# Kernel optimization log

Hardware: AMD Instinct MI355X
Metric: run time of the kernel (lower is better)

Reference implementation:

```python
import jax, jax.numpy as jnp
import numpy as np
from jax import lax

N, H, W, C = 4, 256, 256, 128
COUT = 128
BS_IN, BS_OUT, BSTR = 18, 16, 16  # gather block, conv-out block, block stride
N_ACTIVE = 512


def setup_inputs() -> dict:
    key = jax.random.key(0)
    ks = jax.random.split(key, 8)
    x = jax.random.normal(ks[0], (N, H, W, C), dtype=jnp.float32)
    w = jax.random.normal(ks[1], (3, 3, C, COUT), dtype=jnp.float32) * 0.05  # HWIO
    b = jax.random.normal(ks[2], (COUT,), dtype=jnp.float32) * 0.05
    gamma = jax.random.uniform(ks[3], (COUT,), dtype=jnp.float32, minval=0.5, maxval=1.5)
    beta = jax.random.normal(ks[4], (COUT,), dtype=jnp.float32) * 0.1
    mean = jax.random.normal(ks[5], (COUT,), dtype=jnp.float32) * 0.1
    var = jax.random.uniform(ks[6], (COUT,), dtype=jnp.float32, minval=0.5, maxval=1.5)
    # unique active block ids over the N x (H/16) x (W/16) grid -> disjoint scatter targets
    n_blocks = N * (H // BSTR) * (W // BSTR)
    active = jax.random.permutation(ks[7], n_blocks)[:N_ACTIVE].astype(jnp.int32)
    return {"x": x, "w": w, "b": b, "gamma": gamma, "beta": beta,
            "mean": mean, "var": var, "active": active}


def reference(x, w, b, gamma, beta, mean, var, active):
    n_, h_, w_, c_ = x.shape
    nby, nbx = h_ // BSTR, w_ // BSTR
    bn = active // (nby * nbx)
    rem = active % (nby * nbx)
    by = rem // nbx
    bx = rem % nbx

    # --- sparse_gather: overlapping BS_IN x BS_IN input blocks (zero-pad edges) ---
    pad = BS_IN - BS_OUT
    xp = jnp.pad(x, ((0, 0), (0, pad), (0, pad), (0, 0)))
    Hp, Wp = h_ + pad, w_ + pad
    d_in = jnp.arange(BS_IN, dtype=jnp.int32)
    hs = by[:, None] * BSTR + d_in[None, :]            # [Nb, 18]
    ws = bx[:, None] * BSTR + d_in[None, :]            # [Nb, 18]
    gidx = bn[:, None, None] * (Hp * Wp) + hs[:, :, None] * Wp + ws[:, None, :]
    p = xp.reshape(-1, c_)[gidx]                       # [Nb, 18, 18, C]

    # --- dense conv + BN(eval, eps=1e-3) + ReLU on gathered blocks ---
    q = lax.conv_general_dilated(p, w, window_strides=(1, 1), padding='VALID',
                                 dimension_numbers=('NHWC', 'HWIO', 'NHWC'))
    q = q + b
    q = (q - mean) * (gamma * lax.rsqrt(var + 1e-3)) + beta
    q = jax.nn.relu(q)                                 # [Nb, 16, 16, COUT]

    # --- sparse_scatter: write disjoint BS_OUT blocks back into a copy of x ---
    d_out = jnp.arange(BS_OUT, dtype=jnp.int32)
    hso = by[:, None] * BSTR + d_out[None, :]
    wso = bx[:, None] * BSTR + d_out[None, :]
    sidx = bn[:, None, None] * (h_ * w_) + hso[:, :, None] * w_ + wso[:, None, :]
    y = x.reshape(-1, c_).at[sidx.reshape(-1)].set(q.reshape(-1, q.shape[-1]))
    return y.reshape(n_, h_, w_, c_)
```

## Files before the change

kernel.cpp:

```cpp
#include <hip/hip_runtime.h>
#include <hip/hip_bf16.h>

#define H_ 256
#define W_ 256
#define C_ 128
#define NBPOS 1024
#define NACT 512

typedef __bf16 bf16x8 __attribute__((ext_vector_type(8)));
typedef float f32x4 __attribute__((ext_vector_type(4)));

#define SCALE_OFF 294912
#define SHIFT_OFF 295424
#define INACT_OFF 295936

#define LGKM_BARRIER() do { \
  asm volatile("s_waitcnt lgkmcnt(0)" ::: "memory"); \
  __builtin_amdgcn_s_barrier(); \
  __builtin_amdgcn_sched_barrier(0); \
} while (0)

__global__ void prep_kernel(const float* __restrict__ w, const float* __restrict__ b,
                            const float* __restrict__ gamma, const float* __restrict__ beta,
                            const float* __restrict__ mean, const float* __restrict__ var,
                            const int* __restrict__ active,
                            __bf16* __restrict__ wprep, float* __restrict__ scale,
                            float* __restrict__ shift, int* __restrict__ inact) {
  int blk = blockIdx.x, tid = threadIdx.x;
  if (blk < 576) {
    int o = blk * 256 + tid;
    int j = o & 7, cout = (o >> 3) & 127, k8 = (o >> 10) & 15, tap = o >> 14;
    wprep[o] = (__bf16)w[((size_t)tap * 128 + k8 * 8 + j) * 128 + cout];
    return;
  }
  __shared__ unsigned mask[32];
  __shared__ int cnt;
  if (tid < 32) mask[tid] = 0u;
  if (tid == 0) cnt = 0;
  __syncthreads();
  for (int i = tid; i < NACT; i += 256) {
    int a = active[i];
    atomicOr(&mask[a >> 5], 1u << (a & 31));
  }
  if (tid < 128) {
    float s = gamma[tid] * rsqrtf(var[tid] + 1e-3f);
    scale[tid] = s;
    shift[tid] = (b[tid] - mean[tid]) * s + beta[tid];
  }
  __syncthreads();
  for (int p = tid; p < NBPOS; p += 256) {
    if (!((mask[p >> 5] >> (p & 31)) & 1u)) {
      int q = atomicAdd(&cnt, 1);
      inact[q] = p;
    }
  }
}

__global__ __launch_bounds__(256, 2) void main_kernel(
    const float* __restrict__ x, const __bf16* __restrict__ wprep,
    const float* __restrict__ scale, const float* __restrict__ shift,
    const int* __restrict__ active, const int* __restrict__ inact,
    float* __restrict__ y) {
  __shared__ unsigned char ldsA[324 * 128];
  __shared__ unsigned char ldsB[2][8192];

  const int tid = threadIdx.x;
  const int lane = tid & 63;
  const int wid = tid >> 6;

  const int aid = active[blockIdx.x];
  const int bn = aid >> 8, by = (aid >> 4) & 15, bx = aid & 15;
  const int h0 = by * 16, w0 = bx * 16;
  const float* xb = x + (size_t)bn * (H_ * W_ * C_);

  const int cid = inact[blockIdx.x];
  const size_t cbase4 =
      ((((size_t)(cid >> 8) * H_ + ((cid >> 4) & 15) * 16) * W_ + (cid & 15) * 16) * C_) >> 2;
  const f32x4* __restrict__ xs = (const f32x4*)x;
  f32x4* __restrict__ ys = (f32x4*)y;
  f32x4 cbuf[4];
  auto cidx = [&](int c) -> size_t {
    int lin = (c << 8) + tid;
    return cbase4 + (size_t)(lin >> 9) * (W_ * C_ / 4) + (lin & 511);
  };

  f32x4 acc[4][8];
  f32x4 zero = {0.f, 0.f, 0.f, 0.f};
#pragma unroll
  for (int i = 0; i < 4; ++i)
#pragma unroll
    for (int jj = 0; jj < 8; ++jj) acc[i][jj] = zero;

  const uint4* wp4 = (const uint4*)wprep;
  uint4 t0, t1;
  auto load_t = [&](int u) {
    int ks = u % 18, h = u / 18;
    int tile = ((ks >> 1) << 2) + (h << 1) + (ks & 1);
    t0 = wp4[tile * 512 + tid];
    t1 = wp4[tile * 512 + 256 + tid];
  };
  auto stage = [&](int half) {
    for (int u = tid; u < 324 * 8; u += 256) {
      int s = u >> 3, c8 = u & 7;
      int iy = s / 18, ix = s - iy * 18;
      int hs = h0 + iy, wsp = w0 + ix;
      float4 f0 = make_float4(0.f, 0.f, 0.f, 0.f), f1 = f0;
      if (hs < H_ && wsp < W_) {
        const float* p = xb + (size_t)(hs * W_ + wsp) * C_ + half * 64 + c8 * 8;
        f0 = *(const float4*)p;
        f1 = *(const float4*)(p + 4);
      }
      bf16x8 v;
      v[0] = (__bf16)f0.x; v[1] = (__bf16)f0.y; v[2] = (__bf16)f0.z; v[3] = (__bf16)f0.w;
      v[4] = (__bf16)f1.x; v[5] = (__bf16)f1.y; v[6] = (__bf16)f1.z; v[7] = (__bf16)f1.w;
      int lin = s * 128 + c8 * 16;
      *(bf16x8*)(&ldsA[lin ^ ((s & 7) << 4)]) = v;
    }
  };

  cbuf[0] = xs[cidx(0)];
  cbuf[1] = xs[cidx(1)];
  load_t(0);
  stage(0);
  ((uint4*)ldsB[0])[tid] = t0;
  ((uint4*)ldsB[0])[256 + tid] = t1;
  load_t(1);
  LGKM_BARRIER();

  const int koff = (lane >> 4) * 16;
  const int colb = (lane & 15) * 16;
  const int krow = (lane >> 4) * 2048;

#pragma unroll 4
  for (int u = 0; u < 36; ++u) {
    const int cur = u & 1;

    if (u < 32) __builtin_nontemporal_store(cbuf[u & 3], &ys[cidx(u)]);
    if (u < 30) cbuf[(u + 2) & 3] = xs[cidx(u + 2)];

    if (u < 35) {
      ((uint4*)ldsB[cur ^ 1])[tid] = t0;
      ((uint4*)ldsB[cur ^ 1])[256 + tid] = t1;
      if (u < 34) load_t(u + 2);
    }
    int ks = u % 18;
    int tap = ks >> 1, kch = ks & 1;
    int dyv = tap / 3, dxv = tap - dyv * 3;

    bf16x8 a[4];
#pragma unroll
    for (int mi = 0; mi < 4; ++mi) {
      int srow = (wid * 4 + mi + dyv) * 18 + dxv + (lane & 15);
      int lin = srow * 128 + kch * 64 + koff;
      a[mi] = *(const bf16x8*)(&ldsA[lin ^ ((srow & 7) << 4)]);
    }
    bf16x8 bfr[8];
#pragma unroll
    for (int nb = 0; nb < 8; ++nb)
      bfr[nb] = *(const bf16x8*)(&ldsB[cur][krow + nb * 256 + colb]);
#pragma unroll
    for (int mi = 0; mi < 4; ++mi)
#pragma unroll
      for (int nb = 0; nb < 8; ++nb)
        acc[mi][nb] = __builtin_amdgcn_mfma_f32_16x16x32_bf16(a[mi], bfr[nb], acc[mi][nb], 0, 0, 0);

    LGKM_BARRIER();

    if (u == 17) {
      stage(1);
      LGKM_BARRIER();
    }
  }

  const int colc = lane & 15;
  float sc[8], sh[8];
#pragma unroll
  for (int nb = 0; nb < 8; ++nb) {
    sc[nb] = scale[nb * 16 + colc];
    sh[nb] = shift[nb * 16 + colc];
  }
  float* yb = y + (((size_t)bn * H_ + h0) * W_ + w0) * C_;
#pragma unroll
  for (int mi = 0; mi < 4; ++mi) {
    int oy = wid * 4 + mi;
#pragma unroll
    for (int r = 0; r < 4; ++r) {
      int ox = (lane >> 4) * 4 + r;
      float* yr = yb + ((size_t)oy * W_ + ox) * C_;
#pragma unroll
      for (int nb = 0; nb < 8; ++nb) {
        float v = acc[mi][nb][r] * sc[nb] + sh[nb];
        __builtin_nontemporal_store(fmaxf(v, 0.f), &yr[nb * 16 + colc]);
      }
    }
  }
}

extern "C" void kernel_launch(void* const* d_in, const int* in_sizes, int n_in,
                              void* d_out, int out_size, void* d_ws, size_t ws_size,
                              hipStream_t stream) {
  const float* x     = (const float*)d_in[0];
  const float* w     = (const float*)d_in[1];
  const float* b     = (const float*)d_in[2];
  const float* gamma = (const float*)d_in[3];
  const float* beta  = (const float*)d_in[4];
  const float* mean  = (const float*)d_in[5];
  const float* var   = (const float*)d_in[6];
  const int*   act   = (const int*)d_in[7];
  float* y = (float*)d_out;
  char* ws = (char*)d_ws;
  __bf16* wprep = (__bf16*)ws;
  float* scale = (float*)(ws + SCALE_OFF);
  float* shift = (float*)(ws + SHIFT_OFF);
  int* inact = (int*)(ws + INACT_OFF);

  prep_kernel<<<dim3(577), dim3(256), 0, stream>>>(w, b, gamma, beta, mean, var, act,
                                                   wprep, scale, shift, inact);
  main_kernel<<<dim3(NACT), dim3(256), 0, stream>>>(x, wprep, scale, shift, act, inact, y);
}
```

Baseline: 78.76 us.

## Double the K-chunk per pipeline step to halve barriers in the conv loop

```diff
diff --git a/kernel.cpp b/kernel.cpp
--- a/kernel.cpp
+++ b/kernel.cpp
@@ -62,7 +62,7 @@
     const int* __restrict__ active, const int* __restrict__ inact,
     float* __restrict__ y) {
   __shared__ unsigned char ldsA[324 * 128];
-  __shared__ unsigned char ldsB[2][8192];
+  __shared__ unsigned char ldsB[2][16384];
 
   const int tid = threadIdx.x;
   const int lane = tid & 63;
@@ -92,12 +92,11 @@
     for (int jj = 0; jj < 8; ++jj) acc[i][jj] = zero;
 
   const uint4* wp4 = (const uint4*)wprep;
-  uint4 t0, t1;
-  auto load_t = [&](int u) {
-    int ks = u % 18, h = u / 18;
-    int tile = ((ks >> 1) << 2) + (h << 1) + (ks & 1);
-    t0 = wp4[tile * 512 + tid];
-    t1 = wp4[tile * 512 + 256 + tid];
+  uint4 t[4];
+  auto load_t = [&](int v) {
+    int off = (v % 9) * 2048 + (v / 9) * 1024;
+#pragma unroll
+    for (int q = 0; q < 4; ++q) t[q] = wp4[off + q * 256 + tid];
   };
   auto stage = [&](int half) {
     for (int u = tid; u < 324 * 8; u += 256) {
@@ -118,59 +117,72 @@
     }
   };
 
+  load_t(0);
+  stage(0);
+#pragma unroll
+  for (int q = 0; q < 4; ++q) ((uint4*)ldsB[0])[q * 256 + tid] = t[q];
+  load_t(1);
   cbuf[0] = xs[cidx(0)];
   cbuf[1] = xs[cidx(1)];
-  load_t(0);
-  stage(0);
-  ((uint4*)ldsB[0])[tid] = t0;
-  ((uint4*)ldsB[0])[256 + tid] = t1;
-  load_t(1);
+  cbuf[2] = xs[cidx(2)];
+  cbuf[3] = xs[cidx(3)];
   LGKM_BARRIER();
 
   const int koff = (lane >> 4) * 16;
   const int colb = (lane & 15) * 16;
   const int krow = (lane >> 4) * 2048;
 
-#pragma unroll 4
-  for (int u = 0; u < 36; ++u) {
-    const int cur = u & 1;
-
-    if (u < 32) __builtin_nontemporal_store(cbuf[u & 3], &ys[cidx(u)]);
-    if (u < 30) cbuf[(u + 2) & 3] = xs[cidx(u + 2)];
-
-    if (u < 35) {
-      ((uint4*)ldsB[cur ^ 1])[tid] = t0;
-      ((uint4*)ldsB[cur ^ 1])[256 + tid] = t1;
-      if (u < 34) load_t(u + 2);
-    }
-    int ks = u % 18;
-    int tap = ks >> 1, kch = ks & 1;
-    int dyv = tap / 3, dxv = tap - dyv * 3;
-
-    bf16x8 a[4];
-#pragma unroll
-    for (int mi = 0; mi < 4; ++mi) {
-      int srow = (wid * 4 + mi + dyv) * 18 + dxv + (lane & 15);
-      int lin = srow * 128 + kch * 64 + koff;
-      a[mi] = *(const bf16x8*)(&ldsA[lin ^ ((srow & 7) << 4)]);
-    }
-    bf16x8 bfr[8];
-#pragma unroll
-    for (int nb = 0; nb < 8; ++nb)
-      bfr[nb] = *(const bf16x8*)(&ldsB[cur][krow + nb * 256 + colb]);
-#pragma unroll
-    for (int mi = 0; mi < 4; ++mi)
-#pragma unroll
-      for (int nb = 0; nb < 8; ++nb)
-        acc[mi][nb] = __builtin_amdgcn_mfma_f32_16x16x32_bf16(a[mi], bfr[nb], acc[mi][nb], 0, 0, 0);
-
-    LGKM_BARRIER();
-
-    if (u == 17) {
-      stage(1);
-      LGKM_BARRIER();
-    }
-  }
+#define STEP(u, CUR, SA, SB) do {                                              \
+    if ((u) < 17) {                                                            \
+      _Pragma("unroll")                                                        \
+      for (int q = 0; q < 4; ++q)                                              \
+        ((uint4*)ldsB[(CUR) ^ 1])[q * 256 + tid] = t[q];         \
+    }                                                                          \
+    if ((u) < 16) load_t((u) + 2);               \
+    if ((u) < 16) {                                  \
+      __builtin_nontemporal_store(cbuf[SA], &ys[cidx(2 * (u))]);               \
+      __builtin_nontemporal_store(cbuf[SB], &ys[cidx(2 * (u) + 1)]);           \
+    }                                                                          \
+    if ((u) < 14) {                                 \
+      cbuf[SA] = xs[cidx(2 * (u) + 4)];                                        \
+      cbuf[SB] = xs[cidx(2 * (u) + 5)];                                        \
+    }                                                                          \
+    {                                                                          \
+      int tap = (u) % 9;                                                       \
+      int dyv = tap / 3, dxv = tap - dyv * 3;                                  \
+      _Pragma("unroll")                                                        \
+      for (int kk = 0; kk < 2; ++kk) {                                         \
+        bf16x8 a[4];                                                           \
+        _Pragma("unroll")                                                      \
+        for (int mi = 0; mi < 4; ++mi) {                                       \
+          int srow = (wid * 4 + mi + dyv) * 18 + dxv + (lane & 15);            \
+          int lin = srow * 128 + kk * 64 + koff;                               \
+          a[mi] = *(const bf16x8*)(&ldsA[lin ^ ((srow & 7) << 4)]);            \
+        }                                                                      \
+        bf16x8 bfr[8];                                                         \
+        _Pragma("unroll")                                                      \
+        for (int nb = 0; nb < 8; ++nb)                                         \
+          bfr[nb] = *(const bf16x8*)(&ldsB[CUR][kk * 8192 + krow + nb * 256 + colb]); \
+        _Pragma("unroll")                                                      \
+        for (int mi = 0; mi < 4; ++mi)                                         \
+          _Pragma("unroll")                                                    \
+          for (int nb = 0; nb < 8; ++nb)                                       \
+            acc[mi][nb] = __builtin_amdgcn_mfma_f32_16x16x32_bf16(             \
+                a[mi], bfr[nb], acc[mi][nb], 0, 0, 0);                         \
+      }                                                                        \
+    }                                                                          \
+    LGKM_BARRIER();                                                            \
+    if ((u) == 8) {                            \
+      stage(1);                                                                \
+      LGKM_BARRIER();                                                          \
+    }                                                                          \
+  } while (0)
+
+  for (int up = 0; up < 9; ++up) {
+    STEP(2 * up,     0, 0, 1);
+    STEP(2 * up + 1, 1, 2, 3);
+  }
+#undef STEP
 
   const int colc = lane & 15;
   float sc[8], sh[8];
@@ -190,7 +202,7 @@
 #pragma unroll
       for (int nb = 0; nb < 8; ++nb) {
         float v = acc[mi][nb][r] * sc[nb] + sh[nb];
-        __builtin_nontemporal_store(fmaxf(v, 0.f), &yr[nb * 16 + colc]);
+        yr[nb * 16 + colc] = fmaxf(v, 0.f);
       }
     }
   }
```

Measured after the change: 101.1 us. 28.4% more time.
